# Optimization experiments

Hardware: AMD Instinct MI355X
Metric: run time of the kernel (lower is better)

## Reference

```python
import jax, jax.numpy as jnp
import numpy as np

B, N = 4, 512
C_IN, RES, SR = 256, 7, 2
FC_DIM = 1024
NUM_CLASSES, BOX_DIM, BINS = 3, 6, 12
OUT_CH = NUM_CLASSES * (1 + BOX_DIM + 2 * BINS) + 1  # 94
IMG = 512
STRIDES = (8, 16, 32)


def setup_inputs() -> dict:
    key = jax.random.key(0)
    ks = jax.random.split(key, 12)
    feat_p3 = jax.random.normal(ks[0], (B, C_IN, IMG // 8, IMG // 8), jnp.float32)
    feat_p4 = jax.random.normal(ks[1], (B, C_IN, IMG // 16, IMG // 16), jnp.float32)
    feat_p5 = jax.random.normal(ks[2], (B, C_IN, IMG // 32, IMG // 32), jnp.float32)
    cy = jax.random.uniform(ks[3], (B, N), minval=64.0, maxval=448.0)
    cx = jax.random.uniform(ks[4], (B, N), minval=64.0, maxval=448.0)
    h = jax.random.uniform(ks[5], (B, N), minval=16.0, maxval=120.0)
    w = jax.random.uniform(ks[6], (B, N), minval=16.0, maxval=120.0)
    bbox2d = jnp.stack([cy - h / 2, cx - w / 2, cy + h / 2, cx + w / 2], -1)  # tlbr
    anchors = jnp.stack([cy, cx, h, w], -1)  # (y, x, l, w)
    anchor_id = jax.random.randint(ks[7], (B, N), 0, 9, dtype=jnp.int32)
    flat = C_IN * RES * RES
    fc1_w = jax.random.normal(ks[8], (FC_DIM, flat), jnp.float32) * 0.01
    fc1_b = jnp.zeros((FC_DIM,), jnp.float32)
    bn1_g = jnp.ones((FC_DIM,), jnp.float32)
    bn1_b = jnp.zeros((FC_DIM,), jnp.float32)
    fc2_w = jax.random.normal(ks[9], (FC_DIM, FC_DIM), jnp.float32) * 0.02
    fc2_b = jnp.zeros((FC_DIM,), jnp.float32)
    bn2_g = jnp.ones((FC_DIM,), jnp.float32)
    bn2_b = jnp.zeros((FC_DIM,), jnp.float32)
    pred_w = jax.random.normal(ks[10], (OUT_CH, FC_DIM), jnp.float32) * 0.02
    pred_b = jnp.zeros((OUT_CH,), jnp.float32)
    return dict(feat_p3=feat_p3, feat_p4=feat_p4, feat_p5=feat_p5, bbox2d=bbox2d,
                anchors=anchors, anchor_id=anchor_id, fc1_w=fc1_w, fc1_b=fc1_b,
                bn1_g=bn1_g, bn1_b=bn1_b, fc2_w=fc2_w, fc2_b=fc2_b,
                bn2_g=bn2_g, bn2_b=bn2_b, pred_w=pred_w, pred_b=pred_b)


def _roi_align(feat, boxes, scale):
    # feat: [C,H,W]; boxes: [N,4] tlbr in image coords; aligned=True ROIAlign.
    C, H, W = feat.shape
    S = RES * SR
    t = boxes[:, 0] * scale - 0.5
    l = boxes[:, 1] * scale - 0.5
    bh = (boxes[:, 2] - boxes[:, 0]) * scale / RES  # bin height
    bw = (boxes[:, 3] - boxes[:, 1]) * scale / RES
    g = (jnp.arange(S, dtype=feat.dtype) + 0.5) / SR  # sample offsets in bin units
    ys = t[:, None] + g[None, :] * bh[:, None]  # [N,S]
    xs = l[:, None] + g[None, :] * bw[:, None]
    yc = jnp.clip(ys, 0.0, H - 1.0)
    xc = jnp.clip(xs, 0.0, W - 1.0)
    y0 = jnp.floor(yc)
    x0 = jnp.floor(xc)
    y0i = y0.astype(jnp.int32)
    x0i = x0.astype(jnp.int32)
    y1i = jnp.minimum(y0i + 1, H - 1)
    x1i = jnp.minimum(x0i + 1, W - 1)
    ly = yc - y0
    lx = xc - x0

    def gat(yi, xi):  # -> [C,N,S,S]
        return feat[:, yi[:, :, None], xi[:, None, :]]

    w00 = ((1 - ly)[:, :, None] * (1 - lx)[:, None, :])[None]
    w01 = ((1 - ly)[:, :, None] * lx[:, None, :])[None]
    w10 = (ly[:, :, None] * (1 - lx)[:, None, :])[None]
    w11 = (ly[:, :, None] * lx[:, None, :])[None]
    v = gat(y0i, x0i) * w00 + gat(y0i, x1i) * w01 + gat(y1i, x0i) * w10 + gat(y1i, x1i) * w11
    v = jnp.transpose(v, (1, 0, 2, 3)).reshape(-1, C, RES, SR, RES, SR)
    return v.mean((3, 5))  # [N,C,RES,RES] avg over sampling grid


def _bn_train(x, g, b):
    m = x.mean(0)
    v = x.var(0)
    return (x - m) * jax.lax.rsqrt(v + 1e-5) * g + b


def _forward(feat_p3, feat_p4, feat_p5, bbox2d, anchors, fc1_w, fc1_b, bn1_g, bn1_b,
             fc2_w, fc2_b, bn2_g, bn2_b, pred_w, pred_b, anchor_id):
    feats = (feat_p3, feat_p4, feat_p5)
    lvl = anchor_id // 3  # [B,N] feature-level assignment
    # box_pooler: pool every box at every level, then select its assigned level
    # (equivalent to the torch gather/sort/cat dispatch, in original box order).
    sel = 0.0
    for i, s in enumerate(STRIDES):
        pooled = jax.vmap(lambda f, bx, sc=1.0 / s: _roi_align(f, bx, sc))(feats[i], bbox2d)
        sel = sel + pooled * (lvl == i)[..., None, None, None].astype(pooled.dtype)
    x = sel.reshape(B * N, -1)  # [B*N, C*7*7]
    x = jax.nn.relu(_bn_train(x @ fc1_w.T + fc1_b, bn1_g, bn1_b))
    x = jax.nn.relu(_bn_train(x @ fc2_w.T + fc2_b, bn2_g, bn2_b))
    pred = (x @ pred_w.T + pred_b).reshape(B, N, OUT_CH)
    # decode: slice per-loss channels then apply box deltas per category
    c0 = NUM_CLASSES + 1
    cat = pred[..., :c0]  # [B,N,4]
    b1 = c0 + NUM_CLASSES * BOX_DIM
    bbox3d = pred[..., c0:b1].reshape(B, N, NUM_CLASSES, BOX_DIM)
    yaw_cls = pred[..., b1:b1 + NUM_CLASSES * BINS]
    yaw_res = pred[..., b1 + NUM_CLASSES * BINS:]
    delta = bbox3d[..., :4]  # yxlw deltas per category
    zh = bbox3d[..., 4:]
    stride_px = jnp.exp2(lvl.astype(pred.dtype) + 3.0)  # 8/16/32
    yx = anchors[:, :, None, :2] + delta[..., :2] * stride_px[..., None, None]
    lw = anchors[:, :, None, 2:] * jnp.exp(jnp.clip(delta[..., 2:], -4.0, 4.0))
    box_out = jnp.concatenate([yx, lw, zh], -1).reshape(B, N, NUM_CLASSES * BOX_DIM)
    return jnp.concatenate([cat, box_out, yaw_cls, yaw_res], -1)  # [B,N,94]


def reference(feat_p3, feat_p4, feat_p5, bbox2d, anchors, anchor_id, fc1_w, fc1_b,
              bn1_g, bn1_b, fc2_w, fc2_b, bn2_g, bn2_b, pred_w, pred_b):
    return _forward(feat_p3, feat_p4, feat_p5, bbox2d, anchors, fc1_w, fc1_b, bn1_g,
                    bn1_b, fc2_w, fc2_b, bn2_g, bn2_b, pred_w, pred_b, anchor_id)
```

## Files before the change

kernel.cpp:

```cpp
#include <hip/hip_runtime.h>
#include <hip/hip_bf16.h>

typedef __attribute__((ext_vector_type(8))) short short8;
typedef __attribute__((ext_vector_type(4))) float floatx4;
typedef __attribute__((ext_vector_type(4))) unsigned short ushort4v;

#define DEVI __device__ __forceinline__


DEVI unsigned short f2bf(float v) {
  union { __hip_bfloat16 h; unsigned short u; } cv;
  cv.h = __float2bfloat16(v);
  return cv.u;
}
DEVI short f2bfs(float v) { return (short)f2bf(v); }

DEVI void gload16(const void* gptr, void* lptr) {
  __builtin_amdgcn_global_load_lds(
      (const __attribute__((address_space(1))) unsigned int*)gptr,
      (__attribute__((address_space(3))) unsigned int*)(unsigned long long)(uintptr_t)lptr,
      16, 0, 0);
}

__global__ void cvt_bf16x4_kernel(const float4* __restrict__ src,
                                  ushort4v* __restrict__ dst, size_t n4) {
  size_t i = (size_t)blockIdx.x * blockDim.x + threadIdx.x;
  if (i >= n4) return;
  float4 v = src[i];
  ushort4v o;
  o[0] = f2bf(v.x); o[1] = f2bf(v.y); o[2] = f2bf(v.z); o[3] = f2bf(v.w);
  dst[i] = o;
}

__global__ void cvt_pad_pred_kernel(const float* __restrict__ src,
                                    unsigned short* __restrict__ dst) {
  int i = blockIdx.x * blockDim.x + threadIdx.x;
  if (i >= 96 * 1024) return;
  int row = i >> 10;
  dst[i] = (row < 94) ? f2bf(src[i]) : (unsigned short)0;
}

__global__ __launch_bounds__(256) void roi_mm2_kernel(
    const float* __restrict__ p3, const float* __restrict__ p4,
    const float* __restrict__ p5, const float* __restrict__ bbox,
    const int* __restrict__ aid, unsigned short* __restrict__ X) {
  constexpr int PS = 260;
  __shared__ float P[32 * PS];
  __shared__ float wyx[238];
  __shared__ int sy0[14], sx0[14];
  __shared__ float sly[14], slx[14];

  const int box = blockIdx.x;
  const int oct = blockIdx.y;
  const int b = box >> 9;
  const int tid = threadIdx.x;
  const int lane = tid & 63, wid = tid >> 6;

  const int lvl = aid[box] / 3;
  const int H = 64 >> lvl;
  const int HH = H * H;
  const float* base = (lvl == 0) ? p3 : ((lvl == 1) ? p4 : p5);
  const float scale = 0.125f / (float)(1 << lvl);

  if (tid < 28) {
    int s = tid;
    bool isY = s < 14;
    int k = isY ? s : s - 14;
    float lo = bbox[box * 4 + (isY ? 0 : 1)];
    float hi = bbox[box * 4 + (isY ? 2 : 3)];
    float t = lo * scale - 0.5f;
    float cell = (hi - lo) * scale * (1.0f / 7.0f);
    float pos = t + ((float)k + 0.5f) * 0.5f * cell;
    pos = fminf(fmaxf(pos, 0.0f), (float)(H - 1));
    int i0 = (int)floorf(pos);
    if (i0 > H - 2) i0 = H - 2;
    float fr = pos - (float)i0;
    if (isY) { sy0[k] = i0; sly[k] = fr; }
    else     { sx0[k] = i0; slx[k] = fr; }
  }
  __syncthreads();

  const int ryb = min(sy0[0], H - 16);
  const int rxb = min(sx0[0], H - 16);
  const float* fb = base + ((size_t)b * 256 + oct * 32) * HH + ryb * H + rxb;

  if (tid < 224) {
    int j = tid;
    bool isY = j < 112;
    int k2 = isY ? j : j - 112;
    int py = k2 >> 4, r = k2 & 15;
    int o0 = isY ? ryb : rxb;
    float acc = 0.f;
#pragma unroll
    for (int ss = 0; ss < 2; ++ss) {
      int s = 2 * py + ss;
      int rel = (isY ? sy0[s] : sx0[s]) - o0;
      float fr = isY ? sly[s] : slx[s];
      if (r == rel)     acc += 1.0f - fr;
      if (r == rel + 1) acc += fr;
    }
    wyx[(isY ? 0 : 119) + py * 17 + r] = acc * 0.5f;
  }

  {
    const int r = lane >> 2, c4 = (lane & 3) * 4;
    const float* src0 = fb + r * H + c4;
#pragma unroll
    for (int it = 0; it < 8; ++it) {
      int ch = it * 4 + wid;
      gload16(src0 + (size_t)ch * HH, &P[ch * PS] + lane * 4);
    }
  }
  __syncthreads();

  const int fr = lane & 15, fg = lane >> 4;
  const int chf = wid >> 1;
  const int cellb = (wid & 1) * 32;
  const int cell0 = cellb + fr;
  const int cell1 = cellb + 16 + fr;
  const int py0 = (cell0 * 37) >> 8, px0 = cell0 - py0 * 7;
  const int py1 = (cell1 * 37) >> 8, px1 = cell1 - py1 * 7;
  const float* wyB = wyx;
  const float* wxB = wyx + 119;

  floatx4 acc0 = (floatx4){0.f, 0.f, 0.f, 0.f};
  floatx4 acc1 = (floatx4){0.f, 0.f, 0.f, 0.f};

#pragma unroll
  for (int kk = 0; kk < 8; ++kk) {
    const float* ap = &P[(chf * 16 + fr) * PS + kk * 32 + fg * 8];
    floatx4 a0 = *(const floatx4*)ap;
    floatx4 a1 = *(const floatx4*)(ap + 4);
    short8 af;
    af[0] = f2bfs(a0[0]); af[1] = f2bfs(a0[1]); af[2] = f2bfs(a0[2]); af[3] = f2bfs(a0[3]);
    af[4] = f2bfs(a1[0]); af[5] = f2bfs(a1[1]); af[6] = f2bfs(a1[2]); af[7] = f2bfs(a1[3]);

    const int r = 2 * kk + (fg >> 1);
    const int c0 = (fg & 1) * 8;
    const float w0 = wyB[py0 * 17 + r];
    const float w1 = wyB[py1 * 17 + r];
    const float* x0 = &wxB[px0 * 17 + c0];
    const float* x1 = &wxB[px1 * 17 + c0];
    short8 b0, b1;
#pragma unroll
    for (int e = 0; e < 8; ++e) {
      b0[e] = f2bfs(w0 * x0[e]);
      b1[e] = f2bfs(w1 * x1[e]);
    }
    acc0 = __builtin_amdgcn_mfma_f32_16x16x32_bf16(af, b0, acc0, 0, 0, 0);
    acc1 = __builtin_amdgcn_mfma_f32_16x16x32_bf16(af, b1, acc1, 0, 0, 0);
  }

  unsigned short* xb = X + (size_t)box * 12544 + (size_t)(oct * 32 + chf * 16) * 49;
#pragma unroll
  for (int q = 0; q < 4; ++q)
    xb[(fg * 4 + q) * 49 + cell0] = f2bf(acc0[q]);
  if (cell1 < 49) {
#pragma unroll
    for (int q = 0; q < 4; ++q)
      xb[(fg * 4 + q) * 49 + cell1] = f2bf(acc1[q]);
  }
}

template <int KSPLIT>
__global__ __launch_bounds__(256) void gemm_bt_swz(
    const unsigned short* __restrict__ A, const unsigned short* __restrict__ Bw,
    float* __restrict__ C, int M, int N, int K) {
  constexpr int BM = 128, BN = 128, BK = 64;
  __shared__ unsigned short As[BM * BK];
  __shared__ unsigned short Bs[BN * BK];

  const int tid = threadIdx.x;
  const int lane = tid & 63, wid = tid >> 6;
  const int wr = wid >> 1, wc = wid & 1;
  const int tm = blockIdx.x * BM, tn = blockIdx.y * BN;
  const int fr = lane & 15, fg = lane >> 4;

  const int kLen = K / KSPLIT;
  const int kTiles = kLen / BK;
  const int kBeg = blockIdx.z * kLen;
  float* Cz = C + (size_t)blockIdx.z * M * N;

  floatx4 acc[4][4];
#pragma unroll
  for (int i = 0; i < 4; ++i)
#pragma unroll
    for (int j = 0; j < 4; ++j)
      acc[i][j] = (floatx4){0.f, 0.f, 0.f, 0.f};

  for (int t = 0; t < kTiles; ++t) {
    const int k0 = kBeg + t * BK;
#pragma unroll
    for (int s = tid; s < BM * 8; s += 256) {
      int row = s >> 3, sl = s & 7;
      int slg = sl ^ (row & 7);
      gload16(&A[(size_t)(tm + row) * K + k0 + slg * 8], &As[s * 8]);
    }
#pragma unroll
    for (int s = tid; s < BN * 8; s += 256) {
      int row = s >> 3, sl = s & 7;
      int slg = sl ^ (row & 7);
      gload16(&Bw[(size_t)(tn + row) * K + k0 + slg * 8], &Bs[s * 8]);
    }
    __syncthreads();

#pragma unroll
    for (int kk = 0; kk < 2; ++kk) {
      short8 af[4], bf[4];
#pragma unroll
      for (int i = 0; i < 4; ++i) {
        int row = wr * 64 + i * 16 + fr;
        int sl = (kk * 4 + fg) ^ (row & 7);
        af[i] = *reinterpret_cast<const short8*>(&As[(row * 8 + sl) * 8]);
      }
#pragma unroll
      for (int j = 0; j < 4; ++j) {
        int row = wc * 64 + j * 16 + fr;
        int sl = (kk * 4 + fg) ^ (row & 7);
        bf[j] = *reinterpret_cast<const short8*>(&Bs[(row * 8 + sl) * 8]);
      }
#pragma unroll
      for (int i = 0; i < 4; ++i)
#pragma unroll
        for (int j = 0; j < 4; ++j)
          acc[i][j] = __builtin_amdgcn_mfma_f32_16x16x32_bf16(af[i], bf[j], acc[i][j], 0, 0, 0);
    }
    __syncthreads();
  }

#pragma unroll
  for (int i = 0; i < 4; ++i)
#pragma unroll
    for (int j = 0; j < 4; ++j)
#pragma unroll
      for (int q = 0; q < 4; ++q) {
        int rr = tm + wr * 64 + i * 16 + fg * 4 + q;
        int cc = tn + wc * 64 + j * 16 + fr;
        Cz[(size_t)rr * N + cc] = acc[i][j][q];
      }
}

template <int BM, int BN, int WAVES_M, int WAVES_N, int KSPLIT>
__global__ __launch_bounds__(256) void gemm_bt_kernel(
    const unsigned short* __restrict__ A, const unsigned short* __restrict__ Bw,
    float* __restrict__ C, int M, int N, int K) {
  constexpr int BK = 32;
  constexpr int WM = BM / WAVES_M, WN = BN / WAVES_N;
  constexpr int AF = WM / 16, BF = WN / 16;
  constexpr int ASLOT = BM * 4;
  constexpr int BSLOT = BN * 4;
  __shared__ unsigned short As[BM * BK];
  __shared__ unsigned short Bs[BN * BK];

  const int tid = threadIdx.x;
  const int lane = tid & 63, wid = tid >> 6;
  const int wr = wid / WAVES_N, wc = wid % WAVES_N;
  const int tm = blockIdx.x * BM, tn = blockIdx.y * BN;
  const int fr = lane & 15, fg = lane >> 4;

  const int kLen = K / KSPLIT;
  const int kBeg = blockIdx.z * kLen;
  float* Cz = C + (size_t)blockIdx.z * M * N;

  floatx4 acc[AF][BF];
#pragma unroll
  for (int i = 0; i < AF; ++i)
#pragma unroll
    for (int j = 0; j < BF; ++j)
      acc[i][j] = (floatx4){0.f, 0.f, 0.f, 0.f};

  for (int k0 = kBeg; k0 < kBeg + kLen; k0 += BK) {
#pragma unroll
    for (int s = tid; s < ASLOT; s += 256) {
      int row = s >> 2, kb = (s & 3) << 3;
      gload16(&A[(size_t)(tm + row) * K + k0 + kb], &As[s * 8]);
    }
#pragma unroll
    for (int s = tid; s < BSLOT; s += 256) {
      int row = s >> 2, kb = (s & 3) << 3;
      gload16(&Bw[(size_t)(tn + row) * K + k0 + kb], &Bs[s * 8]);
    }
    __syncthreads();

    short8 af[AF], bfv[BF];
#pragma unroll
    for (int i = 0; i < AF; ++i)
      af[i] = *reinterpret_cast<const short8*>(&As[(wr * WM + i * 16 + fr) * BK + fg * 8]);
#pragma unroll
    for (int j = 0; j < BF; ++j)
      bfv[j] = *reinterpret_cast<const short8*>(&Bs[(wc * WN + j * 16 + fr) * BK + fg * 8]);
#pragma unroll
    for (int i = 0; i < AF; ++i)
#pragma unroll
      for (int j = 0; j < BF; ++j)
        acc[i][j] = __builtin_amdgcn_mfma_f32_16x16x32_bf16(af[i], bfv[j], acc[i][j], 0, 0, 0);
    __syncthreads();
  }

#pragma unroll
  for (int i = 0; i < AF; ++i)
#pragma unroll
    for (int j = 0; j < BF; ++j)
#pragma unroll
      for (int q = 0; q < 4; ++q) {
        int rr = tm + wr * WM + i * 16 + fg * 4 + q;
        int cc = tn + wc * WN + j * 16 + fr;
        Cz[(size_t)rr * N + cc] = acc[i][j][q];
      }
}

__global__ void bn_stats_red_kernel(const float* __restrict__ Yp, float* __restrict__ Yred,
                                    float* __restrict__ psum, float* __restrict__ psq,
                                    int Ncols, int rowsPer, int P, size_t pstride) {
  int c = blockIdx.x * blockDim.x + threadIdx.x;
  int r0 = blockIdx.y * rowsPer;
  float s = 0.f, ss = 0.f;
  for (int r = 0; r < rowsPer; ++r) {
    size_t idx = (size_t)(r0 + r) * Ncols + c;
    float v = Yp[idx];
    for (int p = 1; p < P; ++p) v += Yp[idx + (size_t)p * pstride];
    Yred[idx] = v;
    s += v;
    ss += v * v;
  }
  psum[(size_t)blockIdx.y * Ncols + c] = s;
  psq[(size_t)blockIdx.y * Ncols + c] = ss;
}

__global__ void bn_finalize_kernel(const float* __restrict__ psum, const float* __restrict__ psq,
                                   const float* __restrict__ g, const float* __restrict__ b,
                                   float* __restrict__ scale, float* __restrict__ shift,
                                   int Ncols, int P, float invM) {
  int c = blockIdx.x * blockDim.x + threadIdx.x;
  if (c >= Ncols) return;
  float s = 0.f, ss = 0.f;
  for (int p = 0; p < P; ++p) {
    s += psum[(size_t)p * Ncols + c];
    ss += psq[(size_t)p * Ncols + c];
  }
  float mean = s * invM;
  float var = ss * invM - mean * mean;
  float rstd = rsqrtf(var + 1e-5f);
  float sc = rstd * g[c];
  scale[c] = sc;
  shift[c] = b[c] - mean * sc;
}

__global__ void bn_apply4_kernel(const float4* __restrict__ Y, const float* __restrict__ scale,
                                 const float* __restrict__ shift, ushort4v* __restrict__ X,
                                 int colGroupsMask, int total4) {
  int i = blockIdx.x * blockDim.x + threadIdx.x;
  if (i >= total4) return;
  int c0 = (i & colGroupsMask) * 4;
  float4 v = Y[i];
  ushort4v o;
  o[0] = f2bf(fmaxf(v.x * scale[c0 + 0] + shift[c0 + 0], 0.0f));
  o[1] = f2bf(fmaxf(v.y * scale[c0 + 1] + shift[c0 + 1], 0.0f));
  o[2] = f2bf(fmaxf(v.z * scale[c0 + 2] + shift[c0 + 2], 0.0f));
  o[3] = f2bf(fmaxf(v.w * scale[c0 + 3] + shift[c0 + 3], 0.0f));
  X[i] = o;
}

__global__ void decode_kernel(const float* __restrict__ Y3, const float* __restrict__ pb,
                              const float* __restrict__ anchors, const int* __restrict__ aid,
                              float* __restrict__ out) {
  int i = blockIdx.x * blockDim.x + threadIdx.x;
  if (i >= 2048 * 94) return;
  int bn = i / 94;
  int ch = i - bn * 94;
  size_t idx = (size_t)bn * 96 + ch;
  float v = Y3[idx] + Y3[idx + 2048 * 96] + Y3[idx + 2 * 2048 * 96] + Y3[idx + 3 * 2048 * 96];
  v += pb[ch];
  float o = v;
  if (ch >= 4 && ch < 22) {
    int q = ch - 4;
    int d = q % 6;
    if (d < 2) {
      float stride_px = (float)(8 << (aid[bn] / 3));
      o = anchors[(size_t)bn * 4 + d] + v * stride_px;
    } else if (d < 4) {
      float cl = fminf(fmaxf(v, -4.0f), 4.0f);
      o = anchors[(size_t)bn * 4 + d] * expf(cl);
    }
  }
  out[i] = o;
}

extern "C" void kernel_launch(void* const* d_in, const int* in_sizes, int n_in,
                              void* d_out, int out_size, void* d_ws, size_t ws_size,
                              hipStream_t stream) {
  const float* feat_p3   = (const float*)d_in[0];
  const float* feat_p4   = (const float*)d_in[1];
  const float* feat_p5   = (const float*)d_in[2];
  const float* bbox2d    = (const float*)d_in[3];
  const float* anchors   = (const float*)d_in[4];
  const int*   anchor_id = (const int*)d_in[5];
  const float* fc1_w     = (const float*)d_in[6];
  const float* bn1_g     = (const float*)d_in[8];
  const float* bn1_b     = (const float*)d_in[9];
  const float* fc2_w     = (const float*)d_in[10];
  const float* bn2_g     = (const float*)d_in[12];
  const float* bn2_b     = (const float*)d_in[13];
  const float* pred_w    = (const float*)d_in[14];
  const float* pred_b    = (const float*)d_in[15];
  float* out = (float*)d_out;

  const int M = 2048;
  const int K1 = 12544;
  const int FC = 1024;
  const int RG = 128;

  char* ws = (char*)d_ws;
  auto alloc = [&](size_t bytes) -> char* {
    char* p = ws;
    ws += (bytes + 255) & ~(size_t)255;
    return p;
  };
  unsigned short* W1b  = (unsigned short*)alloc((size_t)FC * K1 * 2);
  unsigned short* W2b  = (unsigned short*)alloc((size_t)FC * FC * 2);
  unsigned short* W3b  = (unsigned short*)alloc((size_t)96 * FC * 2);
  unsigned short* X1   = (unsigned short*)alloc((size_t)M * K1 * 2);
  float*          Yp   = (float*)alloc((size_t)4 * M * FC * 4);
  float*          Yr   = (float*)alloc((size_t)M * FC * 4);
  unsigned short* X2   = (unsigned short*)alloc((size_t)M * FC * 2);
  unsigned short* X3   = (unsigned short*)alloc((size_t)M * FC * 2);
  float*          Y3   = (float*)alloc((size_t)4 * M * 96 * 4);
  float*          ps   = (float*)alloc((size_t)RG * FC * 4);
  float*          pq   = (float*)alloc((size_t)RG * FC * 4);
  float*          sc1  = (float*)alloc((size_t)FC * 4);
  float*          sh1  = (float*)alloc((size_t)FC * 4);
  float*          sc2  = (float*)alloc((size_t)FC * 4);
  float*          sh2  = (float*)alloc((size_t)FC * 4);

  {
    size_t n4 = (size_t)FC * K1 / 4;
    cvt_bf16x4_kernel<<<(unsigned)((n4 + 255) / 256), 256, 0, stream>>>(
        (const float4*)fc1_w, (ushort4v*)W1b, n4);
  }
  {
    size_t n4 = (size_t)FC * FC / 4;
    cvt_bf16x4_kernel<<<(unsigned)((n4 + 255) / 256), 256, 0, stream>>>(
        (const float4*)fc2_w, (ushort4v*)W2b, n4);
  }
  cvt_pad_pred_kernel<<<(96 * 1024) / 256, 256, 0, stream>>>(pred_w, W3b);

  roi_mm2_kernel<<<dim3(2048, 8), 256, 0, stream>>>(feat_p3, feat_p4, feat_p5,
                                                    bbox2d, anchor_id, X1);

  gemm_bt_swz<4><<<dim3(M / 128, FC / 128, 4), 256, 0, stream>>>(X1, W1b, Yp, M, FC, K1);

  bn_stats_red_kernel<<<dim3(FC / 256, RG), 256, 0, stream>>>(Yp, Yr, ps, pq, FC, M / RG, 4, (size_t)M * FC);
  bn_finalize_kernel<<<FC / 256, 256, 0, stream>>>(ps, pq, bn1_g, bn1_b, sc1, sh1, FC, RG, 1.0f / M);
  bn_apply4_kernel<<<(M * FC / 4) / 256, 256, 0, stream>>>(
      (const float4*)Yr, sc1, sh1, (ushort4v*)X2, FC / 4 - 1, M * FC / 4);

  gemm_bt_swz<2><<<dim3(M / 128, FC / 128, 2), 256, 0, stream>>>(X2, W2b, Yp, M, FC, FC);

  bn_stats_red_kernel<<<dim3(FC / 256, RG), 256, 0, stream>>>(Yp, Yr, ps, pq, FC, M / RG, 2, (size_t)M * FC);
  bn_finalize_kernel<<<FC / 256, 256, 0, stream>>>(ps, pq, bn2_g, bn2_b, sc2, sh2, FC, RG, 1.0f / M);
  bn_apply4_kernel<<<(M * FC / 4) / 256, 256, 0, stream>>>(
      (const float4*)Yr, sc2, sh2, (ushort4v*)X3, FC / 4 - 1, M * FC / 4);

  gemm_bt_kernel<64, 96, 2, 2, 4><<<dim3(M / 64, 1, 4), 256, 0, stream>>>(X3, W3b, Y3, M, 96, FC);

  decode_kernel<<<(2048 * 94 + 255) / 256, 256, 0, stream>>>(Y3, pred_b, anchors, anchor_id, out);
}
```

Measured before the change: 256.5 us.

## Issue feature loads early, stage bf16 patch and precomputed bilinear weights in LDS

```diff
diff --git a/kernel.cpp b/kernel.cpp
--- a/kernel.cpp
+++ b/kernel.cpp
@@ -40,12 +40,13 @@
   dst[i] = (row < 94) ? f2bf(src[i]) : (unsigned short)0;
 }
 
-__global__ __launch_bounds__(256) void roi_mm2_kernel(
+__global__ __launch_bounds__(256) void roi_mm3_kernel(
     const float* __restrict__ p3, const float* __restrict__ p4,
     const float* __restrict__ p5, const float* __restrict__ bbox,
     const int* __restrict__ aid, unsigned short* __restrict__ X) {
-  constexpr int PS = 260;
-  __shared__ float P[32 * PS];
+  constexpr int SP = 264;
+  __shared__ unsigned short Pl[32 * SP];
+  __shared__ unsigned short Wl[49 * SP];
   __shared__ float wyx[238];
   __shared__ int sy0[14], sx0[14];
   __shared__ float sly[14], slx[14];
@@ -62,12 +63,41 @@
   const float* base = (lvl == 0) ? p3 : ((lvl == 1) ? p4 : p5);
   const float scale = 0.125f / (float)(1 << lvl);
 
+  const float by0 = bbox[box * 4 + 0], bx0 = bbox[box * 4 + 1];
+  const float by1 = bbox[box * 4 + 2], bx1 = bbox[box * 4 + 3];
+  int ryb, rxb;
+  {
+    float t = by0 * scale - 0.5f;
+    float cell = (by1 - by0) * scale * (1.0f / 7.0f);
+    float pos = t + 0.25f * cell;
+    pos = fminf(fmaxf(pos, 0.0f), (float)(H - 1));
+    int i0 = (int)floorf(pos);
+    if (i0 > H - 2) i0 = H - 2;
+    ryb = min(i0, H - 16);
+    t = bx0 * scale - 0.5f;
+    cell = (bx1 - bx0) * scale * (1.0f / 7.0f);
+    pos = t + 0.25f * cell;
+    pos = fminf(fmaxf(pos, 0.0f), (float)(H - 1));
+    i0 = (int)floorf(pos);
+    if (i0 > H - 2) i0 = H - 2;
+    rxb = min(i0, H - 16);
+  }
+  const float* fb = base + ((size_t)b * 256 + oct * 32) * HH + ryb * H + rxb;
+
+  const int pch = tid & 31, prp = tid >> 5;
+  const float* sr0 = fb + (size_t)pch * HH + (2 * prp) * H;
+  const float* sr1 = sr0 + H;
+  float4 va0 = *(const float4*)(sr0 + 0), va1 = *(const float4*)(sr0 + 4);
+  float4 va2 = *(const float4*)(sr0 + 8), va3 = *(const float4*)(sr0 + 12);
+  float4 vb0 = *(const float4*)(sr1 + 0), vb1 = *(const float4*)(sr1 + 4);
+  float4 vb2 = *(const float4*)(sr1 + 8), vb3 = *(const float4*)(sr1 + 12);
+
   if (tid < 28) {
     int s = tid;
     bool isY = s < 14;
     int k = isY ? s : s - 14;
-    float lo = bbox[box * 4 + (isY ? 0 : 1)];
-    float hi = bbox[box * 4 + (isY ? 2 : 3)];
+    float lo = isY ? by0 : bx0;
+    float hi = isY ? by1 : bx1;
     float t = lo * scale - 0.5f;
     float cell = (hi - lo) * scale * (1.0f / 7.0f);
     float pos = t + ((float)k + 0.5f) * 0.5f * cell;
@@ -80,10 +110,6 @@
   }
   __syncthreads();
 
-  const int ryb = min(sy0[0], H - 16);
-  const int rxb = min(sx0[0], H - 16);
-  const float* fb = base + ((size_t)b * 256 + oct * 32) * HH + ryb * H + rxb;
-
   if (tid < 224) {
     int j = tid;
     bool isY = j < 112;
@@ -103,13 +129,35 @@
   }
 
   {
-    const int r = lane >> 2, c4 = (lane & 3) * 4;
-    const float* src0 = fb + r * H + c4;
-#pragma unroll
-    for (int it = 0; it < 8; ++it) {
-      int ch = it * 4 + wid;
-      gload16(src0 + (size_t)ch * HH, &P[ch * PS] + lane * 4);
-    }
+    unsigned short* pd = &Pl[pch * SP + (2 * prp) * 16];
+    unsigned int d[8];
+    d[0] = f2bf(va0.x) | (f2bf(va0.y) << 16); d[1] = f2bf(va0.z) | (f2bf(va0.w) << 16);
+    d[2] = f2bf(va1.x) | (f2bf(va1.y) << 16); d[3] = f2bf(va1.z) | (f2bf(va1.w) << 16);
+    d[4] = f2bf(va2.x) | (f2bf(va2.y) << 16); d[5] = f2bf(va2.z) | (f2bf(va2.w) << 16);
+    d[6] = f2bf(va3.x) | (f2bf(va3.y) << 16); d[7] = f2bf(va3.z) | (f2bf(va3.w) << 16);
+    *(uint4*)&pd[0] = make_uint4(d[0], d[1], d[2], d[3]);
+    *(uint4*)&pd[8] = make_uint4(d[4], d[5], d[6], d[7]);
+    d[0] = f2bf(vb0.x) | (f2bf(vb0.y) << 16); d[1] = f2bf(vb0.z) | (f2bf(vb0.w) << 16);
+    d[2] = f2bf(vb1.x) | (f2bf(vb1.y) << 16); d[3] = f2bf(vb1.z) | (f2bf(vb1.w) << 16);
+    d[4] = f2bf(vb2.x) | (f2bf(vb2.y) << 16); d[5] = f2bf(vb2.z) | (f2bf(vb2.w) << 16);
+    d[6] = f2bf(vb3.x) | (f2bf(vb3.y) << 16); d[7] = f2bf(vb3.z) | (f2bf(vb3.w) << 16);
+    *(uint4*)&pd[16] = make_uint4(d[0], d[1], d[2], d[3]);
+    *(uint4*)&pd[24] = make_uint4(d[4], d[5], d[6], d[7]);
+  }
+  __syncthreads();
+
+  for (int i = tid; i < 49 * 128; i += 256) {
+    int cell = i >> 7;
+    int d = i & 127;
+    int r = d >> 3;
+    int c = (d & 7) * 2;
+    int py = (cell * 37) >> 8;
+    int px = cell - py * 7;
+    float wyv = wyx[py * 17 + r];
+    const float* wxp = &wyx[119 + px * 17 + c];
+    unsigned int pk = (unsigned int)f2bf(wyv * wxp[0]) |
+                      ((unsigned int)f2bf(wyv * wxp[1]) << 16);
+    *(unsigned int*)&Wl[cell * SP + d * 2] = pk;
   }
   __syncthreads();
 
@@ -118,35 +166,16 @@
   const int cellb = (wid & 1) * 32;
   const int cell0 = cellb + fr;
   const int cell1 = cellb + 16 + fr;
-  const int py0 = (cell0 * 37) >> 8, px0 = cell0 - py0 * 7;
-  const int py1 = (cell1 * 37) >> 8, px1 = cell1 - py1 * 7;
-  const float* wyB = wyx;
-  const float* wxB = wyx + 119;
+  const int crow1 = min(cell1, 48);
 
   floatx4 acc0 = (floatx4){0.f, 0.f, 0.f, 0.f};
   floatx4 acc1 = (floatx4){0.f, 0.f, 0.f, 0.f};
 
 #pragma unroll
   for (int kk = 0; kk < 8; ++kk) {
-    const float* ap = &P[(chf * 16 + fr) * PS + kk * 32 + fg * 8];
-    floatx4 a0 = *(const floatx4*)ap;
-    floatx4 a1 = *(const floatx4*)(ap + 4);
-    short8 af;
-    af[0] = f2bfs(a0[0]); af[1] = f2bfs(a0[1]); af[2] = f2bfs(a0[2]); af[3] = f2bfs(a0[3]);
-    af[4] = f2bfs(a1[0]); af[5] = f2bfs(a1[1]); af[6] = f2bfs(a1[2]); af[7] = f2bfs(a1[3]);
-
-    const int r = 2 * kk + (fg >> 1);
-    const int c0 = (fg & 1) * 8;
-    const float w0 = wyB[py0 * 17 + r];
-    const float w1 = wyB[py1 * 17 + r];
-    const float* x0 = &wxB[px0 * 17 + c0];
-    const float* x1 = &wxB[px1 * 17 + c0];
-    short8 b0, b1;
-#pragma unroll
-    for (int e = 0; e < 8; ++e) {
-      b0[e] = f2bfs(w0 * x0[e]);
-      b1[e] = f2bfs(w1 * x1[e]);
-    }
+    short8 af = *(const short8*)&Pl[(chf * 16 + fr) * SP + kk * 32 + fg * 8];
+    short8 b0 = *(const short8*)&Wl[cell0 * SP + kk * 32 + fg * 8];
+    short8 b1 = *(const short8*)&Wl[crow1 * SP + kk * 32 + fg * 8];
     acc0 = __builtin_amdgcn_mfma_f32_16x16x32_bf16(af, b0, acc0, 0, 0, 0);
     acc1 = __builtin_amdgcn_mfma_f32_16x16x32_bf16(af, b1, acc1, 0, 0, 0);
   }
@@ -444,7 +473,7 @@
   }
   cvt_pad_pred_kernel<<<(96 * 1024) / 256, 256, 0, stream>>>(pred_w, W3b);
 
-  roi_mm2_kernel<<<dim3(2048, 8), 256, 0, stream>>>(feat_p3, feat_p4, feat_p5,
+  roi_mm3_kernel<<<dim3(2048, 8), 256, 0, stream>>>(feat_p3, feat_p4, feat_p5,
                                                     bbox2d, anchor_id, X1);
 
   gemm_bt_swz<4><<<dim3(M / 128, FC / 128, 4), 256, 0, stream>>>(X1, W1b, Yp, M, FC, K1);
```

New measurement: 301.2 us. 1.17x slower.
